# Kernel tuning notes

Measured on AMD Instinct MI355X. Metric: run time of the kernel, lower is better.

The kernel has to match this reference:

```python
import jax, jax.numpy as jnp
import numpy as np

DIM = 1024
NUM_HEADS = 16
HEAD_DIM = DIM // NUM_HEADS
SCALE = 1.0 / float(np.sqrt(HEAD_DIM))


def setup_inputs() -> dict:
    key = jax.random.key(0)
    ks = jax.random.split(key, 5)
    B, S = 2, 2048
    x = jax.random.normal(ks[0], (B, S, DIM), dtype=jnp.float32)
    qkv_w = jax.random.normal(ks[1], (3 * DIM, DIM), dtype=jnp.float32) * (1.0 / np.sqrt(DIM))
    qkv_b = jax.random.normal(ks[2], (3 * DIM,), dtype=jnp.float32) * 0.02
    proj_w = jax.random.normal(ks[3], (DIM, DIM), dtype=jnp.float32) * (1.0 / np.sqrt(DIM))
    proj_b = jax.random.normal(ks[4], (DIM,), dtype=jnp.float32) * 0.02
    return {"x": x, "qkv_w": qkv_w, "qkv_b": qkv_b, "proj_w": proj_w, "proj_b": proj_b}


def reference(x, qkv_w, qkv_b, proj_w, proj_b):
    B, S, _ = x.shape
    # qkv projection: (B,S,3*DIM) -> (3, B, H, S, Dh)
    qkv = x @ qkv_w.T + qkv_b
    qkv = qkv.reshape(B, S, 3, NUM_HEADS, HEAD_DIM).transpose(2, 0, 3, 1, 4)
    q, k, v = qkv[0], qkv[1], qkv[2]
    # scaled dot-product attention (full score matrix, as in the original)
    scores = jnp.einsum('bhqd,bhkd->bhqk', q, k) * SCALE
    attn = jax.nn.softmax(scores, axis=-1)
    out = jnp.einsum('bhqk,bhkd->bhqd', attn, v)  # (B,H,S,Dh)
    out = out.transpose(0, 2, 1, 3).reshape(B, S, DIM)
    return out @ proj_w.T + proj_b
```

## Files before the change

kernel.cpp:

```cpp
#include <hip/hip_runtime.h>

#define DIM_ 1024
#define NH_ 16
#define HD_ 64
#define B_ 2
#define S_ 2048
#define M_ (B_ * S_)
#define NQKV_ (3 * DIM_)

typedef __attribute__((ext_vector_type(8))) __bf16 bf16x8;
typedef __attribute__((ext_vector_type(4))) __bf16 bf16x4;
typedef __attribute__((ext_vector_type(4))) float f32x4;

__device__ __forceinline__ void gl_lds16(const void* g, void* l) {
  __builtin_amdgcn_global_load_lds(
      (__attribute__((address_space(1))) void*)const_cast<void*>(g),
      (__attribute__((address_space(3))) void*)l, 16, 0, 0);
}

#define N4_X 1048576
#define N4_W1 786432
#define N4_W2 262144
__global__ __launch_bounds__(256) void cast_all(const float* __restrict__ x,
                                                const float* __restrict__ w1,
                                                const float* __restrict__ w2,
                                                __bf16* __restrict__ xb,
                                                __bf16* __restrict__ w1b,
                                                __bf16* __restrict__ w2b) {
  int i = blockIdx.x * 256 + threadIdx.x;
  const int stride = gridDim.x * 256;
  for (; i < N4_X + N4_W1 + N4_W2; i += stride) {
    const float4* src;
    bf16x4* dst;
    int j;
    if (i < N4_X) { src = (const float4*)x; dst = (bf16x4*)xb; j = i; }
    else if (i < N4_X + N4_W1) { src = (const float4*)w1; dst = (bf16x4*)w1b; j = i - N4_X; }
    else { src = (const float4*)w2; dst = (bf16x4*)w2b; j = i - (N4_X + N4_W1); }
    float4 v = src[j];
    bf16x4 o;
    o[0] = (__bf16)v.x; o[1] = (__bf16)v.y; o[2] = (__bf16)v.z; o[3] = (__bf16)v.w;
    dst[j] = o;
  }
}

template <int MODE, int BM>
__global__ __launch_bounds__(512, 4) void gemm_bt(const __bf16* __restrict__ A,
                                                  const __bf16* __restrict__ Bw,
                                                  const float* __restrict__ bias,
                                                  __bf16* __restrict__ Qp, __bf16* __restrict__ Kp,
                                                  __bf16* __restrict__ Vt,
                                                  float* __restrict__ Cout) {
  constexpr int KD = 1024;
  constexpr int BN = 128;
  constexpr int MT = BM / 64;
  constexpr int NC = (BM + BN) / 64;
  __shared__ __bf16 As[BM * 64];
  __shared__ __bf16 Bs[BN * 64];
  const int tid = threadIdx.x;
  const int lane = tid & 63;
  const int wave = tid >> 6;
  const int quad = lane >> 4;
  const int r16 = lane & 15;
  const int wm = wave >> 1;
  const int wn = wave & 1;
  const int m0 = blockIdx.y * BM;
  const int n0 = blockIdx.x * BN;

  const f32x4 fz = {0.f, 0.f, 0.f, 0.f};
  f32x4 acc[MT][4];
#pragma unroll
  for (int i = 0; i < MT; ++i)
#pragma unroll
    for (int j = 0; j < 4; ++j) acc[i][j] = fz;

  const __bf16* gp[NC];
  __bf16* lp[NC];
#pragma unroll
  for (int i = 0; i < NC; ++i) {
    const int c = tid + i * 512;
    if (c < BM * 8) {
      const int r = c >> 3, cc = c & 7;
      gp[i] = A + (size_t)(m0 + r) * KD + ((cc ^ (r & 7)) * 8);
      lp[i] = &As[c * 8];
    } else {
      const int c2 = c - BM * 8;
      const int r = c2 >> 3, cc = c2 & 7;
      gp[i] = Bw + (size_t)(n0 + r) * KD + ((cc ^ (r & 7)) * 8);
      lp[i] = &Bs[c2 * 8];
    }
  }

  for (int kt = 0; kt < KD / 64; ++kt) {
    __syncthreads();
#pragma unroll
    for (int i = 0; i < NC; ++i) { gl_lds16(gp[i], lp[i]); gp[i] += 64; }
    __syncthreads();

#pragma unroll
    for (int sub = 0; sub < 2; ++sub) {
      const int ch = ((sub * 4 + quad) ^ (r16 & 7)) * 8;
      bf16x8 af[MT], bfr[4];
#pragma unroll
      for (int mt = 0; mt < MT; ++mt)
        af[mt] = *(const bf16x8*)&As[(wm * MT * 16 + mt * 16 + r16) * 64 + ch];
#pragma unroll
      for (int nt = 0; nt < 4; ++nt)
        bfr[nt] = *(const bf16x8*)&Bs[(wn * 64 + nt * 16 + r16) * 64 + ch];
#pragma unroll
      for (int mt = 0; mt < MT; ++mt)
#pragma unroll
        for (int nt = 0; nt < 4; ++nt)
          acc[mt][nt] =
              __builtin_amdgcn_mfma_f32_16x16x32_bf16(af[mt], bfr[nt], acc[mt][nt], 0, 0, 0);
    }
  }

  if (MODE == 0) {
#pragma unroll
    for (int nt = 0; nt < 4; ++nt) {
      const int n = n0 + wn * 64 + nt * 16 + r16;
      const int sel = n >> 10;
      const int h = (n >> 6) & 15;
      const int dh = n & 63;
      const float bs = bias[n];
      if (sel == 2) {
#pragma unroll
        for (int mt = 0; mt < MT; ++mt) {
          const int m = m0 + wm * MT * 16 + mt * 16 + quad * 4;
          const int b = m >> 11;
          const int s = m & 2047;
          const int slot = (s & ~31) | (((s >> 2) & 3) << 3) | (((s >> 4) & 1) << 2);
          bf16x4 ov;
#pragma unroll
          for (int r = 0; r < 4; ++r) ov[r] = (__bf16)(acc[mt][nt][r] + bs);
          *(bf16x4*)&Vt[((size_t)((b * NH_ + h) * HD_ + dh)) * S_ + slot] = ov;
        }
      } else {
        __bf16* dst = (sel == 0) ? Qp : Kp;
        const float mul = (sel == 0) ? 0.18033688011112042f : 1.0f;
#pragma unroll
        for (int mt = 0; mt < MT; ++mt) {
#pragma unroll
          for (int r = 0; r < 4; ++r) {
            const int m = m0 + wm * MT * 16 + mt * 16 + quad * 4 + r;
            const int b = m >> 11;
            const int s = m & 2047;
            dst[((size_t)((b * NH_ + h) * S_ + s)) * HD_ + dh] =
                (__bf16)((acc[mt][nt][r] + bs) * mul);
          }
        }
      }
    }
  } else {
#pragma unroll
    for (int nt = 0; nt < 4; ++nt) {
      const int n = n0 + wn * 64 + nt * 16 + r16;
      const float bs = bias[n];
#pragma unroll
      for (int mt = 0; mt < MT; ++mt) {
#pragma unroll
        for (int r = 0; r < 4; ++r) {
          const int m = m0 + wm * MT * 16 + mt * 16 + quad * 4 + r;
          Cout[(size_t)m * DIM_ + n] = acc[mt][nt][r] + bs;
        }
      }
    }
  }
}

__global__ __launch_bounds__(256, 2) void attn(const __bf16* __restrict__ Qp,
                                               const __bf16* __restrict__ Kp,
                                               const __bf16* __restrict__ Vtp,
                                               __bf16* __restrict__ ctx) {
  __shared__ __bf16 Ks[2][128 * 64];
  __shared__ __bf16 Vs[2][64 * 128];
  const int tid = threadIdx.x;
  const int lane = tid & 63;
  const int wave = tid >> 6;
  const int quad = lane >> 4;
  const int r16 = lane & 15;

  const int w = blockIdx.y * 16 + blockIdx.x;
  const int bh = (w & 7) + (((w >> 3) >> 4) << 3);
  const int q0 = ((w >> 3) & 15) * 128;

  const __bf16* qg0 = Qp + ((size_t)bh * S_ + (q0 + wave * 32 + r16)) * HD_;
  const __bf16* qg1 = qg0 + 16 * HD_;
  const bf16x8 qa0 = *(const bf16x8*)(qg0 + quad * 8);
  const bf16x8 qa1 = *(const bf16x8*)(qg0 + 32 + quad * 8);
  const bf16x8 qc0 = *(const bf16x8*)(qg1 + quad * 8);
  const bf16x8 qc1 = *(const bf16x8*)(qg1 + 32 + quad * 8);

  const f32x4 fz = {0.f, 0.f, 0.f, 0.f};
  f32x4 o0[4], o1[4];
#pragma unroll
  for (int d = 0; d < 4; ++d) { o0[d] = fz; o1[d] = fz; }
  float ls0 = 0.f, ls1 = 0.f;

  const __bf16* gk[4];
  const __bf16* gv[4];
  int lofs[4];
#pragma unroll
  for (int i = 0; i < 4; ++i) {
    const int c = tid + i * 256;
    const int kr = c >> 3, kc = c & 7;
    gk[i] = Kp + ((size_t)bh * S_ + kr) * HD_ + ((kc ^ (kr & 7)) * 8);
    const int vr = c >> 4, vc = c & 15;
    gv[i] = Vtp + ((size_t)bh * HD_ + vr) * S_ + ((vc ^ (vr & 15)) * 8);
    lofs[i] = c * 8;
  }

#pragma unroll
  for (int i = 0; i < 4; ++i) {
    gl_lds16(gk[i], &Ks[0][lofs[i]]); gk[i] += 128 * HD_;
    gl_lds16(gv[i], &Vs[0][lofs[i]]); gv[i] += 128;
  }

  for (int kt = 0; kt < S_ / 128; ++kt) {
    const int cb = kt & 1;
    __syncthreads();
    if (kt + 1 < S_ / 128) {
#pragma unroll
      for (int i = 0; i < 4; ++i) {
        gl_lds16(gk[i], &Ks[cb ^ 1][lofs[i]]); gk[i] += 128 * HD_;
        gl_lds16(gv[i], &Vs[cb ^ 1][lofs[i]]); gv[i] += 128;
      }
    }

#pragma unroll
    for (int ks = 0; ks < 4; ++ks) {
      const int row0 = ks * 32 + r16;
      const int row1 = row0 + 16;
      const int xa = (quad ^ (r16 & 7)) * 8;
      const int xb = ((4 + quad) ^ (r16 & 7)) * 8;
      const bf16x8 k00 = *(const bf16x8*)&Ks[cb][row0 * 64 + xa];
      const bf16x8 k01 = *(const bf16x8*)&Ks[cb][row0 * 64 + xb];
      const bf16x8 k10 = *(const bf16x8*)&Ks[cb][row1 * 64 + xa];
      const bf16x8 k11 = *(const bf16x8*)&Ks[cb][row1 * 64 + xb];
      f32x4 t00 = fz, t01 = fz, t10 = fz, t11 = fz;
      t00 = __builtin_amdgcn_mfma_f32_16x16x32_bf16(k00, qa0, t00, 0, 0, 0);
      t00 = __builtin_amdgcn_mfma_f32_16x16x32_bf16(k01, qa1, t00, 0, 0, 0);
      t01 = __builtin_amdgcn_mfma_f32_16x16x32_bf16(k10, qa0, t01, 0, 0, 0);
      t01 = __builtin_amdgcn_mfma_f32_16x16x32_bf16(k11, qa1, t01, 0, 0, 0);
      t10 = __builtin_amdgcn_mfma_f32_16x16x32_bf16(k00, qc0, t10, 0, 0, 0);
      t10 = __builtin_amdgcn_mfma_f32_16x16x32_bf16(k01, qc1, t10, 0, 0, 0);
      t11 = __builtin_amdgcn_mfma_f32_16x16x32_bf16(k10, qc0, t11, 0, 0, 0);
      t11 = __builtin_amdgcn_mfma_f32_16x16x32_bf16(k11, qc1, t11, 0, 0, 0);

      bf16x8 pf0, pf1;
#pragma unroll
      for (int r = 0; r < 4; ++r) {
        const float p00 = __builtin_amdgcn_exp2f(t00[r]);
        const float p01 = __builtin_amdgcn_exp2f(t01[r]);
        const float p10 = __builtin_amdgcn_exp2f(t10[r]);
        const float p11 = __builtin_amdgcn_exp2f(t11[r]);
        ls0 += p00 + p01;
        ls1 += p10 + p11;
        pf0[r] = (__bf16)p00; pf0[4 + r] = (__bf16)p01;
        pf1[r] = (__bf16)p10; pf1[4 + r] = (__bf16)p11;
      }

#pragma unroll
      for (int dt = 0; dt < 4; ++dt) {
        const int row = dt * 16 + r16;
        const bf16x8 va = *(const bf16x8*)&Vs[cb][row * 128 + (((4 * ks + quad) ^ r16) * 8)];
        o0[dt] = __builtin_amdgcn_mfma_f32_16x16x32_bf16(va, pf0, o0[dt], 0, 0, 0);
        o1[dt] = __builtin_amdgcn_mfma_f32_16x16x32_bf16(va, pf1, o1[dt], 0, 0, 0);
      }
    }
  }

  ls0 += __shfl_xor(ls0, 16);
  ls0 += __shfl_xor(ls0, 32);
  ls1 += __shfl_xor(ls1, 16);
  ls1 += __shfl_xor(ls1, 32);
  const float inv0 = 1.0f / ls0;
  const float inv1 = 1.0f / ls1;
  const int b = bh >> 4, h = bh & 15;
  const int s0 = q0 + wave * 32 + r16;
  const int s1 = s0 + 16;
#pragma unroll
  for (int dt = 0; dt < 4; ++dt) {
    bf16x4 ov0, ov1;
#pragma unroll
    for (int r = 0; r < 4; ++r) {
      ov0[r] = (__bf16)(o0[dt][r] * inv0);
      ov1[r] = (__bf16)(o1[dt][r] * inv1);
    }
    *(bf16x4*)&ctx[((size_t)(b * S_ + s0)) * DIM_ + h * 64 + dt * 16 + quad * 4] = ov0;
    *(bf16x4*)&ctx[((size_t)(b * S_ + s1)) * DIM_ + h * 64 + dt * 16 + quad * 4] = ov1;
  }
}

extern "C" void kernel_launch(void* const* d_in, const int* in_sizes, int n_in, void* d_out,
                              int out_size, void* d_ws, size_t ws_size, hipStream_t stream) {
  const float* x = (const float*)d_in[0];
  const float* qkv_w = (const float*)d_in[1];
  const float* qkv_b = (const float*)d_in[2];
  const float* proj_w = (const float*)d_in[3];
  const float* proj_b = (const float*)d_in[4];
  float* out = (float*)d_out;

  char* ws = (char*)d_ws;
  __bf16* Xb = (__bf16*)(ws);
  __bf16* Wb = (__bf16*)(ws + 8388608);
  __bf16* Pb = (__bf16*)(ws + 14680064);
  __bf16* Qp = (__bf16*)(ws + 16777216);
  __bf16* Kp = (__bf16*)(ws + 25165824);
  __bf16* Vt = (__bf16*)(ws + 33554432);
  __bf16* Cx = (__bf16*)(ws + 41943040);

  cast_all<<<2048, 256, 0, stream>>>(x, qkv_w, proj_w, Xb, Wb, Pb);
  gemm_bt<0, 128><<<dim3(NQKV_ / 128, M_ / 128), 512, 0, stream>>>(Xb, Wb, qkv_b, Qp, Kp, Vt,
                                                                   nullptr);
  attn<<<dim3(S_ / 128, 32), 256, 0, stream>>>(Qp, Kp, Vt, Cx);
  gemm_bt<1, 64><<<dim3(DIM_ / 128, M_ / 64), 512, 0, stream>>>(Cx, Pb, proj_b, nullptr, nullptr,
                                                                nullptr, out);
}
```

Baseline: 166.8 us.

## Split attention KV range across two wave groups with LDS reduction

Doubles the attention block to 512 threads and splits the key sequence into two halves, each processed by a group of four waves over 64-key tiles. Partial outputs and row sums from the second group are combined through shared memory before normalization and store. This aims to raise wave occupancy and latency hiding for the grid of 512 blocks, at the cost of an extra reduction step, more barriers per tile and smaller tiles per sync.

```diff
diff --git a/kernel.cpp b/kernel.cpp
--- a/kernel.cpp
+++ b/kernel.cpp
@@ -168,23 +168,26 @@
   }
 }
 
-__global__ __launch_bounds__(256, 2) void attn(const __bf16* __restrict__ Qp,
+__global__ __launch_bounds__(512, 4) void attn(const __bf16* __restrict__ Qp,
                                                const __bf16* __restrict__ Kp,
                                                const __bf16* __restrict__ Vtp,
                                                __bf16* __restrict__ ctx) {
-  __shared__ __bf16 Ks[2][128 * 64];
-  __shared__ __bf16 Vs[2][64 * 128];
+  __shared__ alignas(16) char smem[65536];
+  __bf16* KsB = (__bf16*)smem;
+  __bf16* VsB = (__bf16*)(smem + 32768);
   const int tid = threadIdx.x;
   const int lane = tid & 63;
   const int wave = tid >> 6;
   const int quad = lane >> 4;
   const int r16 = lane & 15;
+  const int kh = wave >> 2;
+  const int ww = wave & 3;
 
   const int w = blockIdx.y * 16 + blockIdx.x;
   const int bh = (w & 7) + (((w >> 3) >> 4) << 3);
   const int q0 = ((w >> 3) & 15) * 128;
 
-  const __bf16* qg0 = Qp + ((size_t)bh * S_ + (q0 + wave * 32 + r16)) * HD_;
+  const __bf16* qg0 = Qp + ((size_t)bh * S_ + (q0 + ww * 32 + r16)) * HD_;
   const __bf16* qg1 = qg0 + 16 * HD_;
   const bf16x8 qa0 = *(const bf16x8*)(qg0 + quad * 8);
   const bf16x8 qa1 = *(const bf16x8*)(qg0 + 32 + quad * 8);
@@ -197,46 +200,52 @@
   for (int d = 0; d < 4; ++d) { o0[d] = fz; o1[d] = fz; }
   float ls0 = 0.f, ls1 = 0.f;
 
-  const __bf16* gk[4];
-  const __bf16* gv[4];
-  int lofs[4];
-#pragma unroll
-  for (int i = 0; i < 4; ++i) {
-    const int c = tid + i * 256;
-    const int kr = c >> 3, kc = c & 7;
-    gk[i] = Kp + ((size_t)bh * S_ + kr) * HD_ + ((kc ^ (kr & 7)) * 8);
-    const int vr = c >> 4, vc = c & 15;
-    gv[i] = Vtp + ((size_t)bh * HD_ + vr) * S_ + ((vc ^ (vr & 15)) * 8);
-    lofs[i] = c * 8;
-  }
-
-#pragma unroll
-  for (int i = 0; i < 4; ++i) {
-    gl_lds16(gk[i], &Ks[0][lofs[i]]); gk[i] += 128 * HD_;
-    gl_lds16(gv[i], &Vs[0][lofs[i]]); gv[i] += 128;
-  }
-
-  for (int kt = 0; kt < S_ / 128; ++kt) {
+  const __bf16* gk[2];
+  const __bf16* gv[2];
+  int lk[2], lv[2];
+#pragma unroll
+  for (int i = 0; i < 2; ++i) {
+    const int c = tid + i * 512;
+    const int half = c >> 9;
+    const int r = (c >> 3) & 63;
+    const int cc = c & 7;
+    gk[i] = Kp + ((size_t)bh * S_ + half * 1024 + r) * HD_ + ((cc ^ (r & 7)) * 8);
+    lk[i] = c * 8;
+    gv[i] = Vtp + ((size_t)bh * HD_ + r) * S_ + half * 1024 + ((cc ^ (r & 7)) * 8);
+    lv[i] = c * 8;
+  }
+
+#pragma unroll
+  for (int i = 0; i < 2; ++i) {
+    gl_lds16(gk[i], KsB + lk[i]); gk[i] += 64 * HD_;
+    gl_lds16(gv[i], VsB + lv[i]); gv[i] += 64;
+  }
+
+  constexpr int NT = 1024 / 64;
+  for (int kt = 0; kt < NT; ++kt) {
     const int cb = kt & 1;
     __syncthreads();
-    if (kt + 1 < S_ / 128) {
-#pragma unroll
-      for (int i = 0; i < 4; ++i) {
-        gl_lds16(gk[i], &Ks[cb ^ 1][lofs[i]]); gk[i] += 128 * HD_;
-        gl_lds16(gv[i], &Vs[cb ^ 1][lofs[i]]); gv[i] += 128;
-      }
-    }
-
-#pragma unroll
-    for (int ks = 0; ks < 4; ++ks) {
+    if (kt + 1 < NT) {
+#pragma unroll
+      for (int i = 0; i < 2; ++i) {
+        gl_lds16(gk[i], KsB + (cb ^ 1) * 8192 + lk[i]); gk[i] += 64 * HD_;
+        gl_lds16(gv[i], VsB + (cb ^ 1) * 8192 + lv[i]); gv[i] += 64;
+      }
+    }
+
+    const __bf16* Kt = KsB + cb * 8192 + kh * 4096;
+    const __bf16* Vt2 = VsB + cb * 8192 + kh * 4096;
+
+#pragma unroll
+    for (int ks = 0; ks < 2; ++ks) {
       const int row0 = ks * 32 + r16;
       const int row1 = row0 + 16;
       const int xa = (quad ^ (r16 & 7)) * 8;
       const int xb = ((4 + quad) ^ (r16 & 7)) * 8;
-      const bf16x8 k00 = *(const bf16x8*)&Ks[cb][row0 * 64 + xa];
-      const bf16x8 k01 = *(const bf16x8*)&Ks[cb][row0 * 64 + xb];
-      const bf16x8 k10 = *(const bf16x8*)&Ks[cb][row1 * 64 + xa];
-      const bf16x8 k11 = *(const bf16x8*)&Ks[cb][row1 * 64 + xb];
+      const bf16x8 k00 = *(const bf16x8*)&Kt[row0 * 64 + xa];
+      const bf16x8 k01 = *(const bf16x8*)&Kt[row0 * 64 + xb];
+      const bf16x8 k10 = *(const bf16x8*)&Kt[row1 * 64 + xa];
+      const bf16x8 k11 = *(const bf16x8*)&Kt[row1 * 64 + xb];
       f32x4 t00 = fz, t01 = fz, t10 = fz, t11 = fz;
       t00 = __builtin_amdgcn_mfma_f32_16x16x32_bf16(k00, qa0, t00, 0, 0, 0);
       t00 = __builtin_amdgcn_mfma_f32_16x16x32_bf16(k01, qa1, t00, 0, 0, 0);
@@ -263,7 +272,7 @@
 #pragma unroll
       for (int dt = 0; dt < 4; ++dt) {
         const int row = dt * 16 + r16;
-        const bf16x8 va = *(const bf16x8*)&Vs[cb][row * 128 + (((4 * ks + quad) ^ r16) * 8)];
+        const bf16x8 va = *(const bf16x8*)&Vt2[row * 64 + (((4 * ks + quad) ^ (r16 & 7)) * 8)];
         o0[dt] = __builtin_amdgcn_mfma_f32_16x16x32_bf16(va, pf0, o0[dt], 0, 0, 0);
         o1[dt] = __builtin_amdgcn_mfma_f32_16x16x32_bf16(va, pf1, o1[dt], 0, 0, 0);
       }
@@ -274,21 +283,40 @@
   ls0 += __shfl_xor(ls0, 32);
   ls1 += __shfl_xor(ls1, 16);
   ls1 += __shfl_xor(ls1, 32);
-  const float inv0 = 1.0f / ls0;
-  const float inv1 = 1.0f / ls1;
-  const int b = bh >> 4, h = bh & 15;
-  const int s0 = q0 + wave * 32 + r16;
-  const int s1 = s0 + 16;
-#pragma unroll
-  for (int dt = 0; dt < 4; ++dt) {
-    bf16x4 ov0, ov1;
-#pragma unroll
-    for (int r = 0; r < 4; ++r) {
-      ov0[r] = (__bf16)(o0[dt][r] * inv0);
-      ov1[r] = (__bf16)(o1[dt][r] * inv1);
-    }
-    *(bf16x4*)&ctx[((size_t)(b * S_ + s0)) * DIM_ + h * 64 + dt * 16 + quad * 4] = ov0;
-    *(bf16x4*)&ctx[((size_t)(b * S_ + s1)) * DIM_ + h * 64 + dt * 16 + quad * 4] = ov1;
+
+  __syncthreads();
+  float* xfer = (float*)smem;
+  float* p = xfer + (ww * 64 + lane) * 36;
+  if (kh) {
+    *(f32x4*)(p + 0) = o0[0];  *(f32x4*)(p + 4) = o0[1];
+    *(f32x4*)(p + 8) = o0[2];  *(f32x4*)(p + 12) = o0[3];
+    *(f32x4*)(p + 16) = o1[0]; *(f32x4*)(p + 20) = o1[1];
+    *(f32x4*)(p + 24) = o1[2]; *(f32x4*)(p + 28) = o1[3];
+    p[32] = ls0; p[33] = ls1;
+  }
+  __syncthreads();
+  if (!kh) {
+    o0[0] += *(const f32x4*)(p + 0);  o0[1] += *(const f32x4*)(p + 4);
+    o0[2] += *(const f32x4*)(p + 8);  o0[3] += *(const f32x4*)(p + 12);
+    o1[0] += *(const f32x4*)(p + 16); o1[1] += *(const f32x4*)(p + 20);
+    o1[2] += *(const f32x4*)(p + 24); o1[3] += *(const f32x4*)(p + 28);
+    ls0 += p[32]; ls1 += p[33];
+    const float inv0 = 1.0f / ls0;
+    const float inv1 = 1.0f / ls1;
+    const int b = bh >> 4, h = bh & 15;
+    const int s0 = q0 + ww * 32 + r16;
+    const int s1 = s0 + 16;
+#pragma unroll
+    for (int dt = 0; dt < 4; ++dt) {
+      bf16x4 ov0, ov1;
+#pragma unroll
+      for (int r = 0; r < 4; ++r) {
+        ov0[r] = (__bf16)(o0[dt][r] * inv0);
+        ov1[r] = (__bf16)(o1[dt][r] * inv1);
+      }
+      *(bf16x4*)&ctx[((size_t)(b * S_ + s0)) * DIM_ + h * 64 + dt * 16 + quad * 4] = ov0;
+      *(bf16x4*)&ctx[((size_t)(b * S_ + s1)) * DIM_ + h * 64 + dt * 16 + quad * 4] = ov1;
+    }
   }
 }
 
@@ -313,7 +341,7 @@
   cast_all<<<2048, 256, 0, stream>>>(x, qkv_w, proj_w, Xb, Wb, Pb);
   gemm_bt<0, 128><<<dim3(NQKV_ / 128, M_ / 128), 512, 0, stream>>>(Xb, Wb, qkv_b, Qp, Kp, Vt,
                                                                    nullptr);
-  attn<<<dim3(S_ / 128, 32), 256, 0, stream>>>(Qp, Kp, Vt, Cx);
+  attn<<<dim3(S_ / 128, 32), 512, 0, stream>>>(Qp, Kp, Vt, Cx);
   gemm_bt<1, 64><<<dim3(DIM_ / 128, M_ / 64), 512, 0, stream>>>(Cx, Pb, proj_b, nullptr, nullptr,
                                                                 nullptr, out);
 }
```

After: 164.6 us (median of 2 runs). Within noise of the previous version (-1.4%).
